# Kernel tuning notes

Measured on AMD Instinct MI355X. Metric: run time of the kernel, lower is better.

## Reference

```python
import jax, jax.numpy as jnp
import numpy as np

EPS = 1e-6
NUM_HEADS = 24

def _rmsnorm(x, w):
    # x: [..., D], fp32 math as in FluxRMSNorm
    xf = x.astype(jnp.float32)
    inv = jax.lax.rsqrt(jnp.mean(xf * xf, axis=-1, keepdims=True) + EPS)
    return w * (xf * inv).astype(x.dtype)

def setup_inputs() -> dict:
    key = jax.random.key(0)
    ks = jax.random.split(key, 4)
    B, N, H = 1, 2048, 3072
    D = H // NUM_HEADS
    s_in = 1.0 / np.sqrt(H)
    return {
        "x": jax.random.normal(ks[0], (B, N, H), jnp.float32),
        "Wqkv": jax.random.normal(ks[1], (H, 3 * H), jnp.float32) * s_in,
        "b_qkv": jnp.zeros((3 * H,), jnp.float32),
        "Wproj": jax.random.normal(ks[2], (H, H), jnp.float32) * s_in,
        "q_norm_w": jnp.ones((D,), jnp.float32),
        "k_norm_w": jnp.ones((D,), jnp.float32),
    }

def reference(x, Wqkv, b_qkv, Wproj, q_norm_w, k_norm_w):
    B, N, hidden = x.shape
    nh = NUM_HEADS
    hd = hidden // nh
    scale = hd ** (-0.5)
    qkv = (x @ Wqkv + b_qkv).reshape(B, N, 3, nh, hd)
    q, k, v = qkv[:, :, 0], qkv[:, :, 1], qkv[:, :, 2]  # [B,N,nh,hd]
    q = _rmsnorm(q, q_norm_w)
    k = _rmsnorm(k, k_norm_w)
    # scores: [B,nh,N,N]
    scores = jnp.einsum('bqhd,bkhd->bhqk', q, k) * scale
    attn = jax.nn.softmax(scores, axis=-1)
    out = jnp.einsum('bhqk,bkhd->bqhd', attn, v).reshape(B, N, hidden)
    return out @ Wproj
```

## Files before the change

kernel.cpp:

```cpp
#include <hip/hip_runtime.h>
#include <hip/hip_bf16.h>

using bf16 = __hip_bfloat16;
typedef __attribute__((ext_vector_type(8))) short short8;
typedef __attribute__((ext_vector_type(4))) float f32x4;
typedef unsigned long long ull;

static constexpr int SEQ  = 2048;
static constexpr int HID  = 3072;
static constexpr int NH   = 24;
static constexpr int HD   = 128;
static constexpr int QKVN = 9216;

__device__ __forceinline__ f32x4 mfma_16x16x32(short8 a, short8 b, f32x4 c) {
  return __builtin_amdgcn_mfma_f32_16x16x32_bf16(a, b, c, 0, 0, 0);
}

#define GLOAD_LDS16(g, l) __builtin_amdgcn_global_load_lds(                 \
    (const __attribute__((address_space(1))) void*)(g),                    \
    (__attribute__((address_space(3))) void*)(l), 16, 0, 0)

typedef __attribute__((address_space(3))) const unsigned char lds_cchar;

__device__ __forceinline__ unsigned pack_bf16(float lo, float hi) {
  bf16 l = __float2bfloat16(lo), h = __float2bfloat16(hi);
  return (unsigned)*(unsigned short*)&l | ((unsigned)*(unsigned short*)&h << 16);
}

__global__ __launch_bounds__(256)
void cvt_f32_bf16_vec(const float* __restrict__ src, bf16* __restrict__ dst, int n4) {
  int i = blockIdx.x * 256 + threadIdx.x;
  if (i >= n4) return;
  float4 v = ((const float4*)src)[i];
  ushort4 o;
  bf16 t0 = __float2bfloat16(v.x); o.x = *(unsigned short*)&t0;
  bf16 t1 = __float2bfloat16(v.y); o.y = *(unsigned short*)&t1;
  bf16 t2 = __float2bfloat16(v.z); o.z = *(unsigned short*)&t2;
  bf16 t3 = __float2bfloat16(v.w); o.w = *(unsigned short*)&t3;
  ((ushort4*)dst)[i] = o;
}

__global__ __launch_bounds__(256)
void transpose_cvt64(const float* __restrict__ src, bf16* __restrict__ dst, int R, int C) {
  __shared__ float tile[32][65];
  const int c0 = blockIdx.x * 64, r0 = blockIdx.y * 32;
  const int lc = threadIdx.x & 63, lt = threadIdx.x >> 6;
  #pragma unroll
  for (int i = 0; i < 8; ++i)
    tile[lt + i * 4][lc] = src[(size_t)(r0 + lt + i * 4) * C + c0 + lc];
  __syncthreads();
  const int u = threadIdx.x & 15, dr = threadIdx.x >> 4;
  #pragma unroll
  for (int j = 0; j < 4; ++j) {
    const int cc = dr + j * 16;
    bf16 x0 = __float2bfloat16(tile[u * 2][cc]);
    bf16 x1 = __float2bfloat16(tile[u * 2 + 1][cc]);
    ushort2 o;
    o.x = *(unsigned short*)&x0; o.y = *(unsigned short*)&x1;
    *(ushort2*)&dst[(size_t)(c0 + cc) * R + r0 + u * 2] = o;
  }
}

template<int BIAS>
__global__ __launch_bounds__(768, 3)
void gemm12w(const bf16* __restrict__ A, const bf16* __restrict__ BT,
             const float* __restrict__ bias, bf16* __restrict__ Cout,
             int M, int N, int K) {
  __shared__ __align__(16) bf16 Asb[2][256 * 64];
  __shared__ __align__(16) bf16 Bsb[2][288 * 64];

  const int tid  = threadIdx.x;
  const int lane = tid & 63;
  const int wid  = tid >> 6;
  const int wm   = wid / 6;
  const int wn   = wid % 6;
  const int lr   = lane & 15;
  const int lg   = lane >> 4;

  const int xcd = blockIdx.x & 7;
  const int q   = blockIdx.x >> 3;
  const int bm  = (q & 7) * 256;
  const int bn  = (xcd * 4 + (q >> 3)) * 288;

  const int lrow = lane >> 3;
  const int csrc = ((lane & 7) ^ lrow) * 8;
  const bf16* Abase = A  + (size_t)(bm + lrow) * K + csrc;
  const bf16* Bbase = BT + (size_t)(bn + lrow) * K + csrc;

#define STG12(b, u, i) do {                                                       \
    const int L_ = wid + 12 * (i);                                                \
    if (L_ < 32)      GLOAD_LDS16(Abase + (size_t)(8 * L_) * K + (size_t)(u) * 64,\
                                  &Asb[b][L_ * 512]);                             \
    else if (L_ < 68) GLOAD_LDS16(Bbase + (size_t)(8 * (L_ - 32)) * K + (size_t)(u) * 64, \
                                  &Bsb[b][(L_ - 32) * 512]);                      \
  } while (0)
#define RA12(b, m, kk) (*(const short8*)(&Asb[b][(wm * 128 + (m) * 16 + lr) * 64 \
                          + ((((kk) * 4 + lg)) ^ (lr & 7)) * 8]))
#define RB12(b, n, kk) (*(const short8*)(&Bsb[b][(wn * 48 + (n) * 16 + lr) * 64 \
                          + ((((kk) * 4 + lg)) ^ (lr & 7)) * 8]))

  f32x4 acc[8][3] = {};
  const int NT = K >> 6;

  #pragma unroll
  for (int i = 0; i < 6; ++i) STG12(0, 0, i);

  for (int t = 0; t < NT; ++t) {
    const int c = t & 1, nc = c ^ 1;
    const bool pf = (t + 1) < NT;
    short8 a[4], b[3];

    asm volatile("s_waitcnt vmcnt(0)" ::: "memory");
    __builtin_amdgcn_s_barrier();

    if (pf) {
      STG12(nc, t + 1, 0); STG12(nc, t + 1, 1); STG12(nc, t + 1, 2);
      STG12(nc, t + 1, 3); STG12(nc, t + 1, 4); STG12(nc, t + 1, 5);
    }
    __builtin_amdgcn_sched_barrier(0);

    b[0] = RB12(c, 0, 0); b[1] = RB12(c, 1, 0); b[2] = RB12(c, 2, 0);
    a[0] = RA12(c, 0, 0); a[1] = RA12(c, 1, 0); a[2] = RA12(c, 2, 0); a[3] = RA12(c, 3, 0);
    #pragma unroll
    for (int n = 0; n < 3; ++n)
      #pragma unroll
      for (int m = 0; m < 4; ++m) acc[m][n] = mfma_16x16x32(a[m], b[n], acc[m][n]);

    a[0] = RA12(c, 4, 0); a[1] = RA12(c, 5, 0); a[2] = RA12(c, 6, 0); a[3] = RA12(c, 7, 0);
    #pragma unroll
    for (int n = 0; n < 3; ++n)
      #pragma unroll
      for (int m = 0; m < 4; ++m) acc[4 + m][n] = mfma_16x16x32(a[m], b[n], acc[4 + m][n]);

    b[0] = RB12(c, 0, 1); b[1] = RB12(c, 1, 1); b[2] = RB12(c, 2, 1);
    a[0] = RA12(c, 0, 1); a[1] = RA12(c, 1, 1); a[2] = RA12(c, 2, 1); a[3] = RA12(c, 3, 1);
    #pragma unroll
    for (int n = 0; n < 3; ++n)
      #pragma unroll
      for (int m = 0; m < 4; ++m) acc[m][n] = mfma_16x16x32(a[m], b[n], acc[m][n]);

    a[0] = RA12(c, 4, 1); a[1] = RA12(c, 5, 1); a[2] = RA12(c, 6, 1); a[3] = RA12(c, 7, 1);
    #pragma unroll
    for (int n = 0; n < 3; ++n)
      #pragma unroll
      for (int m = 0; m < 4; ++m) acc[4 + m][n] = mfma_16x16x32(a[m], b[n], acc[4 + m][n]);
  }
#undef STG12
#undef RA12
#undef RB12

  const int row0 = bm + wm * 128 + lg * 4;
  const int col0 = bn + wn * 48 + lr;
  #pragma unroll
  for (int n = 0; n < 3; ++n) {
    const int col = col0 + n * 16;
    const float bv = BIAS ? bias[col] : 0.0f;
    #pragma unroll
    for (int m = 0; m < 8; ++m)
      #pragma unroll
      for (int r = 0; r < 4; ++r)
        Cout[(size_t)(row0 + m * 16 + r) * N + col] = __float2bfloat16(acc[m][n][r] + bv);
  }
}

__global__ __launch_bounds__(256, 2)
void gemm4w(const bf16* __restrict__ A, const bf16* __restrict__ BT,
            float* __restrict__ Cout, int M, int N, int K) {
  __shared__ __align__(16) bf16 Asb[2][128 * 64];
  __shared__ __align__(16) bf16 Bsb[2][96 * 64];

  const int tid  = threadIdx.x;
  const int lane = tid & 63;
  const int wid  = tid >> 6;
  const int wm   = wid >> 1;
  const int wn   = wid & 1;
  const int lr   = lane & 15;
  const int lg   = lane >> 4;

  const int xcd = blockIdx.x & 7;
  const int q   = blockIdx.x >> 3;
  const int bm  = (q & 15) * 128;
  const int bn  = (xcd * 4 + (q >> 4)) * 96;

  const int lrow = lane >> 3;
  const int csrc = ((lane & 7) ^ lrow) * 8;
  const bf16* Abase = A  + (size_t)(bm + lrow) * K + csrc;
  const bf16* Bbase = BT + (size_t)(bn + lrow) * K + csrc;

#define STG4(b, u, i) do {                                                        \
    const int L_ = wid + 4 * (i);                                                 \
    if (L_ < 16)      GLOAD_LDS16(Abase + (size_t)(8 * L_) * K + (size_t)(u) * 64,\
                                  &Asb[b][L_ * 512]);                             \
    else if (L_ < 28) GLOAD_LDS16(Bbase + (size_t)(8 * (L_ - 16)) * K + (size_t)(u) * 64, \
                                  &Bsb[b][(L_ - 16) * 512]);                      \
  } while (0)
#define RA4(b, m, kk) (*(const short8*)(&Asb[b][(wm * 64 + (m) * 16 + lr) * 64 \
                          + ((((kk) * 4 + lg)) ^ (lr & 7)) * 8]))
#define RB4(b, n, kk) (*(const short8*)(&Bsb[b][(wn * 48 + (n) * 16 + lr) * 64 \
                          + ((((kk) * 4 + lg)) ^ (lr & 7)) * 8]))

  f32x4 acc[4][3] = {};
  const int NT = K >> 6;

  #pragma unroll
  for (int i = 0; i < 7; ++i) STG4(0, 0, i);

  for (int t = 0; t < NT; ++t) {
    const int c = t & 1, nc = c ^ 1;
    const bool pf = (t + 1) < NT;
    short8 a[4], b[3];

    asm volatile("s_waitcnt vmcnt(0)" ::: "memory");
    __builtin_amdgcn_s_barrier();

    if (pf) {
      STG4(nc, t + 1, 0); STG4(nc, t + 1, 1); STG4(nc, t + 1, 2); STG4(nc, t + 1, 3);
      STG4(nc, t + 1, 4); STG4(nc, t + 1, 5); STG4(nc, t + 1, 6);
    }
    __builtin_amdgcn_sched_barrier(0);

    b[0] = RB4(c, 0, 0); b[1] = RB4(c, 1, 0); b[2] = RB4(c, 2, 0);
    a[0] = RA4(c, 0, 0); a[1] = RA4(c, 1, 0); a[2] = RA4(c, 2, 0); a[3] = RA4(c, 3, 0);
    #pragma unroll
    for (int n = 0; n < 3; ++n)
      #pragma unroll
      for (int m = 0; m < 4; ++m) acc[m][n] = mfma_16x16x32(a[m], b[n], acc[m][n]);

    b[0] = RB4(c, 0, 1); b[1] = RB4(c, 1, 1); b[2] = RB4(c, 2, 1);
    a[0] = RA4(c, 0, 1); a[1] = RA4(c, 1, 1); a[2] = RA4(c, 2, 1); a[3] = RA4(c, 3, 1);
    #pragma unroll
    for (int n = 0; n < 3; ++n)
      #pragma unroll
      for (int m = 0; m < 4; ++m) acc[m][n] = mfma_16x16x32(a[m], b[n], acc[m][n]);
  }
#undef STG4
#undef RA4
#undef RB4

  const int row0 = bm + wm * 64 + lg * 4;
  const int col0 = bn + wn * 48 + lr;
  #pragma unroll
  for (int n = 0; n < 3; ++n) {
    const int col = col0 + n * 16;
    #pragma unroll
    for (int m = 0; m < 4; ++m)
      #pragma unroll
      for (int r = 0; r < 4; ++r)
        Cout[(size_t)(row0 + m * 16 + r) * N + col] = acc[m][n][r];
  }
}

__global__ __launch_bounds__(256)
void rmsnorm_qk(bf16* __restrict__ qkv, const float* __restrict__ qw,
                const float* __restrict__ kw) {
  const int row  = blockIdx.x * 4 + (threadIdx.x >> 6);
  const int lane = threadIdx.x & 63;
  const int token = row / 48;
  const int rem   = row - token * 48;
  const int which = rem / 24;
  const int head  = rem - which * 24;
  bf16* p = qkv + (long)token * QKVN + which * HID + head * HD;
  const float a = __bfloat162float(p[lane * 2]);
  const float b = __bfloat162float(p[lane * 2 + 1]);
  float ss = a * a + b * b;
  #pragma unroll
  for (int mask = 32; mask >= 1; mask >>= 1) ss += __shfl_xor(ss, mask);
  const float inv = rsqrtf(ss * (1.0f / 128.0f) + 1e-6f);
  const float* w = which ? kw : qw;
  p[lane * 2]     = __float2bfloat16(a * inv * w[lane * 2]);
  p[lane * 2 + 1] = __float2bfloat16(b * inv * w[lane * 2 + 1]);
}

__global__ __launch_bounds__(256, 3)
void attn_kernel(const bf16* __restrict__ qkv, bf16* __restrict__ ctx) {
  const int head = blockIdx.y;
  const int qb   = blockIdx.x;
  const int tid  = threadIdx.x;
  const int lane = tid & 63;
  const int wid  = tid >> 6;
  const int lr   = lane & 15;
  const int lg   = lane >> 4;

  __shared__ __align__(16) unsigned char Ksb[64 * 256];
  __shared__ __align__(16) unsigned char Vsb[128 * 128];
  __shared__ __align__(16) unsigned short Ps[4][16 * 72];

  const int qrow0 = qb * 64 + wid * 16;
  short8 qf[4];
  #pragma unroll
  for (int kt = 0; kt < 4; ++kt)
    qf[kt] = *(const short8*)(qkv + (long)(qrow0 + lr) * QKVN + head * HD + kt * 32 + lg * 8);

  f32x4 oacc[8] = {};
  float mrun = -1e30f, lsum = 0.0f;

  const float scale = 0.088388347648318447f;

  const int stok = tid >> 4;
  const int sdc  = tid & 15;

  short8 kreg[4], vreg[4];
  #pragma unroll
  for (int j = 0; j < 4; ++j) {
    const int tok = stok + (j & 1) * 16 + (j >> 1) * 32;
    kreg[j] = *(const short8*)(qkv + (long)tok * QKVN + HID     + head * HD + sdc * 8);
    vreg[j] = *(const short8*)(qkv + (long)tok * QKVN + 2 * HID + head * HD + sdc * 8);
  }

#define TRISSUE(S, dtv) {                                                         \
    lds_cchar* pd_ = vb0 + (dtv) * 2048;                                          \
    asm volatile("ds_read_b64_tr_b16 %0, %1 offset:0"    : "=v"(S##0) : "v"(pd_));\
    asm volatile("ds_read_b64_tr_b16 %0, %1 offset:512"  : "=v"(S##1) : "v"(pd_));\
    asm volatile("ds_read_b64_tr_b16 %0, %1 offset:1024" : "=v"(S##2) : "v"(pd_));\
    asm volatile("ds_read_b64_tr_b16 %0, %1 offset:1536" : "=v"(S##3) : "v"(pd_));}
#define TRMFMA(S, dtv) {                                                          \
    short8 v0_, v1_;                                                              \
    ((ull*)&v0_)[0] = S##0; ((ull*)&v0_)[1] = S##1;                               \
    ((ull*)&v1_)[0] = S##2; ((ull*)&v1_)[1] = S##3;                               \
    oacc[dtv] = mfma_16x16x32(pa[0], v0_, oacc[dtv]);                             \
    oacc[dtv] = mfma_16x16x32(pa[1], v1_, oacc[dtv]); }
#define TRWAIT4 asm volatile("s_waitcnt lgkmcnt(4)" ::: "memory"); \
                __builtin_amdgcn_sched_barrier(0);

  for (int t = 0; t < SEQ / 64; ++t) {
    __syncthreads();
    #pragma unroll
    for (int j = 0; j < 4; ++j) {
      const int tok = stok + (j & 1) * 16 + (j >> 1) * 32;
      const int dc  = sdc;
      *(short8*)(Ksb + ((tok * 256 + dc * 16) ^ ((tok & 7) << 4))) = kreg[j];
      const int dg = dc >> 1, h = dc & 1, kg = tok >> 2, kr = tok & 3;
      const int pos = (kg & 8) | ((kg & 1) << 2) | ((kg >> 1) & 3);
      *(short8*)(Vsb + (dg * 16 + pos) * 128 + kr * 32 + h * 16) = vreg[j];
    }
    __syncthreads();

    if (t + 1 < SEQ / 64) {
      const int kv1 = (t + 1) * 64;
      #pragma unroll
      for (int j = 0; j < 4; ++j) {
        const int tok = kv1 + stok + (j & 1) * 16 + (j >> 1) * 32;
        kreg[j] = *(const short8*)(qkv + (long)tok * QKVN + HID     + head * HD + sdc * 8);
        vreg[j] = *(const short8*)(qkv + (long)tok * QKVN + 2 * HID + head * HD + sdc * 8);
      }
      __builtin_amdgcn_sched_barrier(0);
    }

    f32x4 st[4];
    __builtin_amdgcn_s_setprio(1);
    #pragma unroll
    for (int ct = 0; ct < 4; ++ct) {
      f32x4 a = {};
      #pragma unroll
      for (int kt = 0; kt < 4; ++kt) {
        short8 kb = *(const short8*)(Ksb +
            ((((ct * 16 + lr) * 256) + kt * 64 + lg * 16) ^ ((lr & 7) << 4)));
        a = mfma_16x16x32(kb, qf[kt], a);
      }
      st[ct] = a;
    }
    __builtin_amdgcn_s_setprio(0);

    float pm = st[0][0];
    #pragma unroll
    for (int ct = 0; ct < 4; ++ct)
      #pragma unroll
      for (int r = 0; r < 4; ++r) pm = fmaxf(pm, st[ct][r]);
    pm *= scale;
    pm = fmaxf(pm, __shfl_xor(pm, 16));
    pm = fmaxf(pm, __shfl_xor(pm, 32));

    if (!__all(pm <= mrun + 8.0f)) {
      const float mnew = fmaxf(mrun, pm);
      const float corr = __expf(mrun - mnew);
      mrun = mnew;
      lsum *= corr;
      #pragma unroll
      for (int r = 0; r < 4; ++r) {
        const float cr = __shfl(corr, lg * 4 + r);
        #pragma unroll
        for (int dt = 0; dt < 8; ++dt) oacc[dt][r] *= cr;
      }
    }

    float ps = 0.0f;
    #pragma unroll
    for (int ct = 0; ct < 4; ++ct) {
      const float p0 = __expf(st[ct][0] * scale - mrun);
      const float p1 = __expf(st[ct][1] * scale - mrun);
      const float p2 = __expf(st[ct][2] * scale - mrun);
      const float p3 = __expf(st[ct][3] * scale - mrun);
      ps += (p0 + p1) + (p2 + p3);
      uint2 w;
      w.x = pack_bf16(p0, p1);
      w.y = pack_bf16(p2, p3);
      *(uint2*)&Ps[wid][lr * 72 + ct * 16 + lg * 4] = w;
    }
    lsum += ps;

    short8 pa[2];
    pa[0] = *(const short8*)&Ps[wid][lr * 72 + lg * 8];
    pa[1] = *(const short8*)&Ps[wid][lr * 72 + 32 + lg * 8];
    __builtin_amdgcn_sched_barrier(0);

    lds_cchar* vb0 = (lds_cchar*)Vsb + lane * 8;
    ull x0, x1, x2, x3, y0, y1, y2, y3;
    __builtin_amdgcn_s_setprio(1);
    TRISSUE(x, 0)
    TRISSUE(y, 1)
    TRWAIT4  TRMFMA(x, 0)  TRISSUE(x, 2)
    TRWAIT4  TRMFMA(y, 1)  TRISSUE(y, 3)
    TRWAIT4  TRMFMA(x, 2)  TRISSUE(x, 4)
    TRWAIT4  TRMFMA(y, 3)  TRISSUE(y, 5)
    TRWAIT4  TRMFMA(x, 4)  TRISSUE(x, 6)
    TRWAIT4  TRMFMA(y, 5)  TRISSUE(y, 7)
    TRWAIT4  TRMFMA(x, 6)
    asm volatile("s_waitcnt lgkmcnt(0)" ::: "memory");
    __builtin_amdgcn_sched_barrier(0);
    TRMFMA(y, 7)
    __builtin_amdgcn_s_setprio(0);
  }
#undef TRISSUE
#undef TRMFMA
#undef TRWAIT4

  lsum += __shfl_xor(lsum, 16);
  lsum += __shfl_xor(lsum, 32);
  const float invl = 1.0f / lsum;
  #pragma unroll
  for (int r = 0; r < 4; ++r) {
    const float inv = __shfl(invl, lg * 4 + r);
    const long tok = qrow0 + lg * 4 + r;
    #pragma unroll
    for (int dt = 0; dt < 8; ++dt)
      ctx[tok * HID + head * HD + dt * 16 + lr] = __float2bfloat16(oacc[dt][r] * inv);
  }
}

extern "C" void kernel_launch(void* const* d_in, const int* in_sizes, int n_in,
                              void* d_out, int out_size, void* d_ws, size_t ws_size,
                              hipStream_t stream) {
  (void)in_sizes; (void)n_in; (void)out_size; (void)ws_size;
  const float* x     = (const float*)d_in[0];
  const float* Wqkv  = (const float*)d_in[1];
  const float* bqkv  = (const float*)d_in[2];
  const float* Wproj = (const float*)d_in[3];
  const float* qw    = (const float*)d_in[4];
  const float* kw    = (const float*)d_in[5];

  char* ws = (char*)d_ws;
  bf16* xb     = (bf16*)ws;
  bf16* WqkvT  = (bf16*)(ws + 12582912);
  bf16* WprojT = (bf16*)(ws + 69206016);
  bf16* qkv    = (bf16*)(ws + 88080384);
  bf16* ctx    = xb;

  cvt_f32_bf16_vec<<<(SEQ * HID / 4 + 255) / 256, 256, 0, stream>>>(x, xb, SEQ * HID / 4);
  transpose_cvt64<<<dim3(QKVN / 64, HID / 32), 256, 0, stream>>>(Wqkv, WqkvT, HID, QKVN);
  transpose_cvt64<<<dim3(HID / 64, HID / 32), 256, 0, stream>>>(Wproj, WprojT, HID, HID);

  gemm12w<1><<<256, 768, 0, stream>>>(xb, WqkvT, bqkv, qkv, SEQ, QKVN, HID);

  rmsnorm_qk<<<SEQ * 48 / 4, 256, 0, stream>>>(qkv, qw, kw);

  attn_kernel<<<dim3(SEQ / 64, NH), 256, 0, stream>>>(qkv, ctx);

  gemm4w<<<512, 256, 0, stream>>>(ctx, WprojT, (float*)d_out, SEQ, HID, HID);
}
```

Measured before the change: 313.8 us.

## Fuse Q RMSNorm into attention and reshape QKV GEMM warp tiling

Q normalization moves into the attention kernel: each wave normalizes its Q fragment in registers right after loading it, so the standalone norm kernel handles only K and does half the read/write traffic. Separately, the 12-wave QKV GEMM is re-tiled from a 2x6 warp grid of 128x48 per wave to a 4x3 grid of 64x96 per wave. This changes the balance between A and B fragment LDS reads per MFMA and shortens the unrolled inner sequence. Q's sum of squares is now computed from bf16 values, matching the previous path, and the per-block Q norm is redone once per K/V sweep at small cost.

```diff
diff --git a/kernel.cpp b/kernel.cpp
--- a/kernel.cpp
+++ b/kernel.cpp
@@ -25,6 +25,12 @@
 __device__ __forceinline__ unsigned pack_bf16(float lo, float hi) {
   bf16 l = __float2bfloat16(lo), h = __float2bfloat16(hi);
   return (unsigned)*(unsigned short*)&l | ((unsigned)*(unsigned short*)&h << 16);
+}
+__device__ __forceinline__ float bfbits2f(short s) {
+  union { float f; unsigned u; } x; x.u = (unsigned)(unsigned short)s << 16; return x.f;
+}
+__device__ __forceinline__ short f2bfbits(float f) {
+  bf16 b = __float2bfloat16(f); return *(short*)&b;
 }
 
 __global__ __launch_bounds__(256)
@@ -72,8 +78,8 @@
   const int tid  = threadIdx.x;
   const int lane = tid & 63;
   const int wid  = tid >> 6;
-  const int wm   = wid / 6;
-  const int wn   = wid % 6;
+  const int wmm  = wid & 3;
+  const int wnn  = wid >> 2;
   const int lr   = lane & 15;
   const int lg   = lane >> 4;
 
@@ -94,12 +100,12 @@
     else if (L_ < 68) GLOAD_LDS16(Bbase + (size_t)(8 * (L_ - 32)) * K + (size_t)(u) * 64, \
                                   &Bsb[b][(L_ - 32) * 512]);                      \
   } while (0)
-#define RA12(b, m, kk) (*(const short8*)(&Asb[b][(wm * 128 + (m) * 16 + lr) * 64 \
+#define RA12(b, m, kk) (*(const short8*)(&Asb[b][(wmm * 64 + (m) * 16 + lr) * 64 \
                           + ((((kk) * 4 + lg)) ^ (lr & 7)) * 8]))
-#define RB12(b, n, kk) (*(const short8*)(&Bsb[b][(wn * 48 + (n) * 16 + lr) * 64 \
+#define RB12(b, n, kk) (*(const short8*)(&Bsb[b][(wnn * 96 + (n) * 16 + lr) * 64 \
                           + ((((kk) * 4 + lg)) ^ (lr & 7)) * 8]))
 
-  f32x4 acc[8][3] = {};
+  f32x4 acc[4][6] = {};
   const int NT = K >> 6;
 
   #pragma unroll
@@ -108,7 +114,7 @@
   for (int t = 0; t < NT; ++t) {
     const int c = t & 1, nc = c ^ 1;
     const bool pf = (t + 1) < NT;
-    short8 a[4], b[3];
+    short8 a[4], b[6];
 
     asm volatile("s_waitcnt vmcnt(0)" ::: "memory");
     __builtin_amdgcn_s_barrier();
@@ -120,43 +126,33 @@
     __builtin_amdgcn_sched_barrier(0);
 
     b[0] = RB12(c, 0, 0); b[1] = RB12(c, 1, 0); b[2] = RB12(c, 2, 0);
+    b[3] = RB12(c, 3, 0); b[4] = RB12(c, 4, 0); b[5] = RB12(c, 5, 0);
     a[0] = RA12(c, 0, 0); a[1] = RA12(c, 1, 0); a[2] = RA12(c, 2, 0); a[3] = RA12(c, 3, 0);
     #pragma unroll
-    for (int n = 0; n < 3; ++n)
+    for (int n = 0; n < 6; ++n)
       #pragma unroll
       for (int m = 0; m < 4; ++m) acc[m][n] = mfma_16x16x32(a[m], b[n], acc[m][n]);
 
-    a[0] = RA12(c, 4, 0); a[1] = RA12(c, 5, 0); a[2] = RA12(c, 6, 0); a[3] = RA12(c, 7, 0);
-    #pragma unroll
-    for (int n = 0; n < 3; ++n)
-      #pragma unroll
-      for (int m = 0; m < 4; ++m) acc[4 + m][n] = mfma_16x16x32(a[m], b[n], acc[4 + m][n]);
-
     b[0] = RB12(c, 0, 1); b[1] = RB12(c, 1, 1); b[2] = RB12(c, 2, 1);
+    b[3] = RB12(c, 3, 1); b[4] = RB12(c, 4, 1); b[5] = RB12(c, 5, 1);
     a[0] = RA12(c, 0, 1); a[1] = RA12(c, 1, 1); a[2] = RA12(c, 2, 1); a[3] = RA12(c, 3, 1);
     #pragma unroll
-    for (int n = 0; n < 3; ++n)
+    for (int n = 0; n < 6; ++n)
       #pragma unroll
       for (int m = 0; m < 4; ++m) acc[m][n] = mfma_16x16x32(a[m], b[n], acc[m][n]);
-
-    a[0] = RA12(c, 4, 1); a[1] = RA12(c, 5, 1); a[2] = RA12(c, 6, 1); a[3] = RA12(c, 7, 1);
-    #pragma unroll
-    for (int n = 0; n < 3; ++n)
-      #pragma unroll
-      for (int m = 0; m < 4; ++m) acc[4 + m][n] = mfma_16x16x32(a[m], b[n], acc[4 + m][n]);
   }
 #undef STG12
 #undef RA12
 #undef RB12
 
-  const int row0 = bm + wm * 128 + lg * 4;
-  const int col0 = bn + wn * 48 + lr;
-  #pragma unroll
-  for (int n = 0; n < 3; ++n) {
+  const int row0 = bm + wmm * 64 + lg * 4;
+  const int col0 = bn + wnn * 96 + lr;
+  #pragma unroll
+  for (int n = 0; n < 6; ++n) {
     const int col = col0 + n * 16;
     const float bv = BIAS ? bias[col] : 0.0f;
     #pragma unroll
-    for (int m = 0; m < 8; ++m)
+    for (int m = 0; m < 4; ++m)
       #pragma unroll
       for (int r = 0; r < 4; ++r)
         Cout[(size_t)(row0 + m * 16 + r) * N + col] = __float2bfloat16(acc[m][n][r] + bv);
@@ -251,28 +247,25 @@
 }
 
 __global__ __launch_bounds__(256)
-void rmsnorm_qk(bf16* __restrict__ qkv, const float* __restrict__ qw,
-                const float* __restrict__ kw) {
+void rmsnorm_k(bf16* __restrict__ qkv, const float* __restrict__ kw) {
   const int row  = blockIdx.x * 4 + (threadIdx.x >> 6);
   const int lane = threadIdx.x & 63;
-  const int token = row / 48;
-  const int rem   = row - token * 48;
-  const int which = rem / 24;
-  const int head  = rem - which * 24;
-  bf16* p = qkv + (long)token * QKVN + which * HID + head * HD;
+  const int token = row / 24;
+  const int head  = row - token * 24;
+  bf16* p = qkv + (size_t)token * QKVN + HID + head * HD;
   const float a = __bfloat162float(p[lane * 2]);
   const float b = __bfloat162float(p[lane * 2 + 1]);
   float ss = a * a + b * b;
   #pragma unroll
   for (int mask = 32; mask >= 1; mask >>= 1) ss += __shfl_xor(ss, mask);
   const float inv = rsqrtf(ss * (1.0f / 128.0f) + 1e-6f);
-  const float* w = which ? kw : qw;
-  p[lane * 2]     = __float2bfloat16(a * inv * w[lane * 2]);
-  p[lane * 2 + 1] = __float2bfloat16(b * inv * w[lane * 2 + 1]);
+  p[lane * 2]     = __float2bfloat16(a * inv * kw[lane * 2]);
+  p[lane * 2 + 1] = __float2bfloat16(b * inv * kw[lane * 2 + 1]);
 }
 
 __global__ __launch_bounds__(256, 3)
-void attn_kernel(const bf16* __restrict__ qkv, bf16* __restrict__ ctx) {
+void attn_kernel(const bf16* __restrict__ qkv, const float* __restrict__ qw,
+                 bf16* __restrict__ ctx) {
   const int head = blockIdx.y;
   const int qb   = blockIdx.x;
   const int tid  = threadIdx.x;
@@ -289,7 +282,26 @@
   short8 qf[4];
   #pragma unroll
   for (int kt = 0; kt < 4; ++kt)
-    qf[kt] = *(const short8*)(qkv + (long)(qrow0 + lr) * QKVN + head * HD + kt * 32 + lg * 8);
+    qf[kt] = *(const short8*)(qkv + (size_t)(qrow0 + lr) * QKVN + head * HD + kt * 32 + lg * 8);
+
+  {
+    float ssq = 0.0f;
+    #pragma unroll
+    for (int kt = 0; kt < 4; ++kt)
+      #pragma unroll
+      for (int j = 0; j < 8; ++j) {
+        const float v = bfbits2f(qf[kt][j]);
+        ssq += v * v;
+      }
+    ssq += __shfl_xor(ssq, 16);
+    ssq += __shfl_xor(ssq, 32);
+    const float qinv = rsqrtf(ssq * (1.0f / 128.0f) + 1e-6f);
+    #pragma unroll
+    for (int kt = 0; kt < 4; ++kt)
+      #pragma unroll
+      for (int j = 0; j < 8; ++j)
+        qf[kt][j] = f2bfbits(bfbits2f(qf[kt][j]) * qinv * qw[kt * 32 + lg * 8 + j]);
+  }
 
   f32x4 oacc[8] = {};
   float mrun = -1e30f, lsum = 0.0f;
@@ -303,8 +315,8 @@
   #pragma unroll
   for (int j = 0; j < 4; ++j) {
     const int tok = stok + (j & 1) * 16 + (j >> 1) * 32;
-    kreg[j] = *(const short8*)(qkv + (long)tok * QKVN + HID     + head * HD + sdc * 8);
-    vreg[j] = *(const short8*)(qkv + (long)tok * QKVN + 2 * HID + head * HD + sdc * 8);
+    kreg[j] = *(const short8*)(qkv + (size_t)tok * QKVN + HID     + head * HD + sdc * 8);
+    vreg[j] = *(const short8*)(qkv + (size_t)tok * QKVN + 2 * HID + head * HD + sdc * 8);
   }
 
 #define TRISSUE(S, dtv) {                                                         \
@@ -340,8 +352,8 @@
       #pragma unroll
       for (int j = 0; j < 4; ++j) {
         const int tok = kv1 + stok + (j & 1) * 16 + (j >> 1) * 32;
-        kreg[j] = *(const short8*)(qkv + (long)tok * QKVN + HID     + head * HD + sdc * 8);
-        vreg[j] = *(const short8*)(qkv + (long)tok * QKVN + 2 * HID + head * HD + sdc * 8);
+        kreg[j] = *(const short8*)(qkv + (size_t)tok * QKVN + HID     + head * HD + sdc * 8);
+        vreg[j] = *(const short8*)(qkv + (size_t)tok * QKVN + 2 * HID + head * HD + sdc * 8);
       }
       __builtin_amdgcn_sched_barrier(0);
     }
@@ -430,7 +442,7 @@
   #pragma unroll
   for (int r = 0; r < 4; ++r) {
     const float inv = __shfl(invl, lg * 4 + r);
-    const long tok = qrow0 + lg * 4 + r;
+    const size_t tok = qrow0 + lg * 4 + r;
     #pragma unroll
     for (int dt = 0; dt < 8; ++dt)
       ctx[tok * HID + head * HD + dt * 16 + lr] = __float2bfloat16(oacc[dt][r] * inv);
@@ -461,9 +473,9 @@
 
   gemm12w<1><<<256, 768, 0, stream>>>(xb, WqkvT, bqkv, qkv, SEQ, QKVN, HID);
 
-  rmsnorm_qk<<<SEQ * 48 / 4, 256, 0, stream>>>(qkv, qw, kw);
-
-  attn_kernel<<<dim3(SEQ / 64, NH), 256, 0, stream>>>(qkv, ctx);
+  rmsnorm_k<<<SEQ * NH / 4, 256, 0, stream>>>(qkv, kw);
+
+  attn_kernel<<<dim3(SEQ / 64, NH), 256, 0, stream>>>(qkv, qw, ctx);
 
   gemm4w<<<512, 256, 0, stream>>>(ctx, WprojT, (float*)d_out, SEQ, HID, HID);
 }
```

Result: slower. 320.4 us (+2.1%).
